# Optimization experiments

Measured on AMD Instinct MI355X. Metric: run time of the kernel, lower is better.

## Reference

```python
import jax, jax.numpy as jnp
import numpy as np

N_NODES = 50000
DEG = 16                      # uniform in-degree so every node receives messages (matches dgl mailbox semantics)
N_EDGES = N_NODES * DEG       # 800000
IND = 128
EDIM = 64
OUT = 128
AVG_D = float(np.log(DEG + 1.0))   # PNA avg_d['log']
EPS = 1e-5


def setup_inputs() -> dict:
    key = jax.random.key(0)
    k = jax.random.split(key, 6)
    h = jax.random.normal(k[0], (N_NODES, IND), dtype=jnp.float32)
    ef = jax.random.normal(k[1], (N_EDGES, EDIM), dtype=jnp.float32)
    src = jax.random.randint(k[2], (N_EDGES,), 0, N_NODES)
    dst = jnp.repeat(jnp.arange(N_NODES), DEG)  # every node has exactly DEG incoming edges
    pre_in = 2 * IND + EDIM            # 320
    post_in = IND * (1 + 4 * 3)        # 1664: h + 4 aggregators x 3 scalers
    W_pre = jax.random.normal(k[3], (pre_in, IND), dtype=jnp.float32) * (1.0 / np.sqrt(pre_in))
    b_pre = jnp.zeros((IND,), dtype=jnp.float32)
    W_post = jax.random.normal(k[4], (post_in, OUT), dtype=jnp.float32) * (1.0 / np.sqrt(post_in))
    b_post = jnp.zeros((OUT,), dtype=jnp.float32)
    return {"h": h, "ef": ef, "src": src, "dst": dst,
            "W_pre": W_pre, "b_pre": b_pre, "W_post": W_post, "b_post": b_post}


def reference(h, ef, src, dst, W_pre, b_pre, W_post, b_post):
    n = h.shape[0]
    # --- pretrans on edges: cat(src_h, dst_h, ef) -> Linear ---
    z2 = jnp.concatenate([h[src], h[dst], ef], axis=1)          # [E, 2*IND+EDIM]
    e = z2 @ W_pre + b_pre                                       # [E, IND]
    # --- multi-aggregator segment reduce over incoming edges (by dst) ---
    deg = jax.ops.segment_sum(jnp.ones((e.shape[0],), e.dtype), dst, num_segments=n)  # [N]
    safe_deg = jnp.maximum(deg, 1.0)[:, None]
    s1 = jax.ops.segment_sum(e, dst, num_segments=n)
    s2 = jax.ops.segment_sum(e * e, dst, num_segments=n)
    mean = s1 / safe_deg
    std = jnp.sqrt(jax.nn.relu(s2 / safe_deg - mean * mean) + EPS)
    mx = jax.ops.segment_max(e, dst, num_segments=n)
    mn = jax.ops.segment_min(e, dst, num_segments=n)
    has = (deg > 0)[:, None]
    mx = jnp.where(has, mx, 0.0)
    mn = jnp.where(has, mn, 0.0)
    agg = jnp.concatenate([mean, mx, mn, std], axis=1)           # [N, 4*IND]
    # --- scalers: identity, amplification log(D+1)/avg_d, attenuation avg_d/log(D+1) ---
    logd = jnp.log(deg + 1.0)
    amp = (logd / AVG_D)[:, None]
    att = (AVG_D / jnp.maximum(logd, 1e-6))[:, None]
    att = jnp.where(deg[:, None] > 0, att, 0.0)
    scaled = jnp.concatenate([agg, agg * amp, agg * att], axis=1)  # [N, 12*IND]
    # --- posttrans on nodes: cat(h, aggregated) -> Linear ---
    hcat = jnp.concatenate([h, scaled], axis=1)                  # [N, 13*IND]
    return hcat @ W_post + b_post                                # [N, OUT]
```

## Files before the change

kernel.cpp:

```cpp
#include <hip/hip_runtime.h>

#define N_NODES 50000
#define IND 128
#define EDIM 64

typedef __bf16 bf16x8 __attribute__((ext_vector_type(8)));
typedef float  f32x4  __attribute__((ext_vector_type(4)));
typedef unsigned short u16x8 __attribute__((ext_vector_type(8)));

__device__ __forceinline__ unsigned short f2bfu(float f) {
  __bf16 b = (__bf16)f;
  return __builtin_bit_cast(unsigned short, b);
}
__device__ __forceinline__ float bfu2f(unsigned short u) {
  __bf16 b = __builtin_bit_cast(__bf16, u);
  return (float)b;
}
__device__ __forceinline__ f32x4 mfma16(bf16x8 a, bf16x8 b, f32x4 c) {
  return __builtin_amdgcn_mfma_f32_16x16x32_bf16(a, b, c, 0, 0, 0);
}
__device__ __forceinline__ bf16x8 pack8(float4 a, float4 b) {
  bf16x8 r;
  r[0]=(__bf16)a.x; r[1]=(__bf16)a.y; r[2]=(__bf16)a.z; r[3]=(__bf16)a.w;
  r[4]=(__bf16)b.x; r[5]=(__bf16)b.y; r[6]=(__bf16)b.z; r[7]=(__bf16)b.w;
  return r;
}

__global__ __launch_bounds__(256) void pack_all(const float* W_pre, const float* W_post,
                                                const float* b_pre, const float* b_post,
                                                unsigned short* WpreF, unsigned short* WcF,
                                                unsigned short* WfoldF, float* bias2) {
  __shared__ float ldsW[16384];
  int b = blockIdx.x, t = threadIdx.x;
  if (b < 16) {
    for (int i = 0; i < 64; i++) {
      int idx = t + i * 256;
      int c = idx >> 7, col = idx & 127;
      float s = 0.f;
#pragma unroll
      for (int sc = 0; sc < 3; sc++)
#pragma unroll
      for (int st = 0; st < 3; st++)
          s += W_post[(size_t)(128 + sc * 512 + st * 128 + c) * 128 + col];
      ldsW[idx] = s;
    }
    __syncthreads();
    int col = t & 127, kh = t >> 7;
    for (int i = 0; i < 4; i++) {
      int k = b * 8 + i * 2 + kh;
      float a0 = W_post[(size_t)k * 128 + col], a1 = 0.f, a2 = 0.f, a3 = 0.f;
      const float* wb = W_pre + (size_t)(128 + k) * 128;
#pragma unroll 4
      for (int c = 0; c < 128; c += 4) {
        a0 = fmaf(wb[c],     ldsW[c * 128 + col], a0);
        a1 = fmaf(wb[c + 1], ldsW[(c + 1) * 128 + col], a1);
        a2 = fmaf(wb[c + 2], ldsW[(c + 2) * 128 + col], a2);
        a3 = fmaf(wb[c + 3], ldsW[(c + 3) * 128 + col], a3);
      }
      float acc = (a0 + a1) + (a2 + a3);
      int kb = k >> 5, j = k & 7, qq = (k >> 3) & 3;
      int lane = qq * 16 + (col & 15), ct = col >> 4;
      WfoldF[((size_t)(kb * 8 + ct) * 64 + lane) * 8 + j] = f2bfu(acc);
    }
    if (b == 0 && t < 128) {
      int col = t;
      float acc = b_post[col];
      for (int c = 0; c < 128; c++) acc = fmaf(b_pre[c], ldsW[c * 128 + col], acc);
      bias2[col] = acc;
    }
  } else {
    int idx = (b - 16) * 256 + t;
    if (idx < 16384) {
      int j = idx & 7, lane = (idx >> 3) & 63, ct = (idx >> 9) & 7, kb = idx >> 12;
      int k = kb * 32 + (lane >> 4) * 8 + j;
      int col = ct * 16 + (lane & 15);
      WpreF[idx] = f2bfu(W_pre[k * 128 + col]);
    } else if (idx < 24576) {
      int i = idx - 16384;
      int j = i & 7, lane = (i >> 3) & 63, ct = (i >> 9) & 7, kb = i >> 12;
      int k = kb * 32 + (lane >> 4) * 8 + j;
      int col = ct * 16 + (lane & 15);
      WcF[i] = f2bfu(W_pre[(256 + k) * 128 + col]);
    } else if (idx < 24576 + 65536) {
      int i = idx - 24576;
      int j = i & 7, lane = (i >> 3) & 63, ct = (i >> 9) & 7, kbr = i >> 12;
      int kb = kbr + 4;
      int p = kbr * 32 + ((lane >> 4) & 3) * 8 + j;
      int tt = p >> 7;
      int c = (p & 7) * 16 + ((p >> 3) & 15);
      int col = ct * 16 + (lane & 15);
      size_t r0 = 128 + (size_t)tt * 128 + c;
      float v = W_post[r0 * 128 + col] + W_post[(r0 + 512) * 128 + col] +
                W_post[(r0 + 1024) * 128 + col];
      WfoldF[((size_t)(kb * 8 + ct) * 64 + lane) * 8 + j] = f2bfu(v);
    }
  }
}

__global__ __launch_bounds__(256) void pre_gemm(const float* h, const unsigned short* WpreF,
                                                unsigned short* haB) {
  int lane = threadIdx.x & 63;
  int gw = blockIdx.x * 4 + (threadIdx.x >> 6);
  size_t base = (size_t)gw * 16;
  if (base >= N_NODES) return;
  int q = lane >> 4, c16 = lane & 15;
  f32x4 acc[8];
#pragma unroll
  for (int i = 0; i < 8; i++) acc[i] = (f32x4){0.f, 0.f, 0.f, 0.f};
#pragma unroll
  for (int kb = 0; kb < 4; kb++) {
    const float* hp = h + (base + c16) * 128 + kb * 32 + q * 8;
    float4 lo = *(const float4*)hp;
    float4 hi = *(const float4*)(hp + 4);
    bf16x8 a = pack8(lo, hi);
#pragma unroll
    for (int ct = 0; ct < 8; ct++) {
      bf16x8 b = *(const bf16x8*)(WpreF + ((size_t)(kb * 8 + ct) * 64 + lane) * 8);
      acc[ct] = mfma16(a, b, acc[ct]);
    }
  }
#pragma unroll
  for (int r = 0; r < 4; r++) {
    size_t row = base + q * 4 + r;
    u16x8 hv;
#pragma unroll
    for (int ct = 0; ct < 8; ct++) hv[ct] = f2bfu(acc[ct][r]);
    *(u16x8*)(haB + row * 128 + c16 * 8) = hv;
  }
}

__device__ __forceinline__ void node_stats(const f32x4* acc, const u16x8* G,
                                           int q, unsigned short* outp) {
  u16x8 ov;
#pragma unroll
  for (int ct = 0; ct < 8; ct++) {
    float sum = 0.f, s2 = 0.f, mx = -3.4e38f, mn = 3.4e38f;
#pragma unroll
    for (int r = 0; r < 4; r++) {
      float e = acc[ct][r] + bfu2f(G[r][ct]);
      sum += e; s2 = __builtin_fmaf(e, e, s2);
      mx = fmaxf(mx, e); mn = fminf(mn, e);
    }
    sum += __shfl_xor(sum, 16, 64); s2 += __shfl_xor(s2, 16, 64);
    mx = fmaxf(mx, __shfl_xor(mx, 16, 64)); mn = fminf(mn, __shfl_xor(mn, 16, 64));
    sum += __shfl_xor(sum, 32, 64); s2 += __shfl_xor(s2, 32, 64);
    mx = fmaxf(mx, __shfl_xor(mx, 32, 64)); mn = fminf(mn, __shfl_xor(mn, 32, 64));
    float mean = sum * 0.0625f;
    float var = fmaxf(s2 * 0.0625f - mean * mean, 0.f);
    float sd = sqrtf(var + 1e-5f);
    float v = (q == 0) ? mean : (q == 1) ? mx : (q == 2) ? mn : sd;
    ov[ct] = f2bfu(v);
  }
  *(u16x8*)outp = ov;
}

__global__ __launch_bounds__(512, 4) void edge_post(const float* ef, const int* src,
                                                    const unsigned short* haB,
                                                    const unsigned short* WcF,
                                                    const float* h,
                                                    const unsigned short* WfoldF,
                                                    const float* bias2, float* out) {
  __shared__ unsigned short ldsWc[8192];
  __shared__ unsigned short sAgg[16 * 512];
  {
    const int4* g = (const int4*)WcF;
    int4* l = (int4*)ldsWc;
#pragma unroll
    for (int i = 0; i < 2; i++) l[threadIdx.x + i * 512] = g[threadIdx.x + i * 512];
  }
  int lane = threadIdx.x & 63, wib = threadIdx.x >> 6;
  int q = lane >> 4, c16 = lane & 15;
  int pr = blockIdx.x * 8 + wib;
  int n0 = pr * 2;
  int srcv = src[pr * 32 + (lane & 31)];
  const float* ep0 = ef + ((size_t)n0 * 16 + c16) * 64 + q * 8;
  float4 E0a = *(const float4*)ep0;
  float4 E0b = *(const float4*)(ep0 + 4);
  float4 E0c = *(const float4*)(ep0 + 32);
  float4 E0d = *(const float4*)(ep0 + 36);
  const float* ep1 = ep0 + 1024;
  float4 E1a = *(const float4*)ep1;
  float4 E1b = *(const float4*)(ep1 + 4);
  float4 E1c = *(const float4*)(ep1 + 32);
  float4 E1d = *(const float4*)(ep1 + 36);
  u16x8 G0[4], G1[4];
#pragma unroll
  for (int r = 0; r < 4; r++) {
    int s = __shfl(srcv, q * 4 + r, 64);
    G0[r] = *(const u16x8*)(haB + (size_t)s * 128 + c16 * 8);
  }
#pragma unroll
  for (int r = 0; r < 4; r++) {
    int s = __shfl(srcv, 16 + q * 4 + r, 64);
    G1[r] = *(const u16x8*)(haB + (size_t)s * 128 + c16 * 8);
  }
  __syncthreads();
  {
    bf16x8 a0 = pack8(E0a, E0b), a1 = pack8(E0c, E0d);
    f32x4 acc[8];
#pragma unroll
    for (int ct = 0; ct < 8; ct++) {
      bf16x8 b = *(const bf16x8*)(ldsWc + ((size_t)ct * 64 + lane) * 8);
      acc[ct] = mfma16(a0, b, (f32x4){0.f, 0.f, 0.f, 0.f});
    }
#pragma unroll
    for (int ct = 0; ct < 8; ct++) {
      bf16x8 b = *(const bf16x8*)(ldsWc + ((size_t)(8 + ct) * 64 + lane) * 8);
      acc[ct] = mfma16(a1, b, acc[ct]);
    }
    node_stats(acc, G0, q, sAgg + (size_t)(wib * 2) * 512 + lane * 8);
  }
  {
    bf16x8 a0 = pack8(E1a, E1b), a1 = pack8(E1c, E1d);
    f32x4 acc[8];
#pragma unroll
    for (int ct = 0; ct < 8; ct++) {
      bf16x8 b = *(const bf16x8*)(ldsWc + ((size_t)ct * 64 + lane) * 8);
      acc[ct] = mfma16(a0, b, (f32x4){0.f, 0.f, 0.f, 0.f});
    }
#pragma unroll
    for (int ct = 0; ct < 8; ct++) {
      bf16x8 b = *(const bf16x8*)(ldsWc + ((size_t)(8 + ct) * 64 + lane) * 8);
      acc[ct] = mfma16(a1, b, acc[ct]);
    }
    node_stats(acc, G1, q, sAgg + (size_t)(wib * 2 + 1) * 512 + lane * 8);
  }
  __syncthreads();
  size_t base = (size_t)blockIdx.x * 16;
  size_t r0 = base + c16;
  f32x4 acc = (f32x4){0.f, 0.f, 0.f, 0.f};
  float4 fa, fb;
  {
    const float* p = h + r0 * 128 + q * 8;
    fa = *(const float4*)p; fb = *(const float4*)(p + 4);
  }
  bf16x8 Bc = *(const bf16x8*)(WfoldF + ((size_t)wib * 64 + lane) * 8);
#pragma unroll
  for (int kb = 0; kb < 20; kb++) {
    bf16x8 a;
    if (kb < 4) {
      a = pack8(fa, fb);
      if (kb < 3) {
        const float* p = h + r0 * 128 + (kb + 1) * 32 + q * 8;
        fa = *(const float4*)p; fb = *(const float4*)(p + 4);
      }
    } else {
      a = *(const bf16x8*)(sAgg + (size_t)c16 * 512 + (kb - 4) * 32 + q * 8);
    }
    bf16x8 Bn = Bc;
    if (kb < 19)
      Bn = *(const bf16x8*)(WfoldF + ((size_t)((kb + 1) * 8 + wib) * 64 + lane) * 8);
    acc = mfma16(a, Bc, acc);
    Bc = Bn;
  }
  int col = wib * 16 + c16;
  float bp = bias2[col];
#pragma unroll
  for (int r = 0; r < 4; r++) {
    size_t row = base + q * 4 + r;
    out[row * 128 + col] = acc[r] + bp;
  }
}

extern "C" void kernel_launch(void* const* d_in, const int* in_sizes, int n_in,
                              void* d_out, int out_size, void* d_ws, size_t ws_size,
                              hipStream_t stream) {
  const float* h      = (const float*)d_in[0];
  const float* ef     = (const float*)d_in[1];
  const int*   src    = (const int*)d_in[2];
  const float* W_pre  = (const float*)d_in[4];
  const float* b_pre  = (const float*)d_in[5];
  const float* W_post = (const float*)d_in[6];
  const float* b_post = (const float*)d_in[7];
  float* out = (float*)d_out;

  char* ws = (char*)d_ws;
  unsigned short* haB    = (unsigned short*)ws;
  unsigned short* WpreF  = haB + (size_t)N_NODES * 128;
  unsigned short* WcF    = WpreF + 16384;
  unsigned short* WfoldF = WcF + 8192;
  float*          bias2  = (float*)(WfoldF + 81920);
  (void)in_sizes; (void)n_in; (void)out_size; (void)ws_size;

  pack_all<<<368, 256, 0, stream>>>(W_pre, W_post, b_pre, b_post, WpreF, WcF, WfoldF, bias2);
  pre_gemm<<<782, 256, 0, stream>>>(h, WpreF, haB);
  edge_post<<<3125, 512, 0, stream>>>(ef, src, haB, WcF, h, WfoldF, bias2, out);
}
```

Measured before the change: 397.5 us.

## Use permlane swaps for node stats, swizzle aggregate LDS, vectorize src loads

Replaces the shuffle-based cross-lane reductions in node_stats with permlane32/permlane16 swap builtins. It packs sum/sumsq and max/negated-min into shared exchanges so fewer cross-lane operations are issued. The aggregate buffer in LDS is re-laid out with an XOR swizzle so the posttrans reads avoid bank conflicts. Source indices now come from vectorized int4 loads instead of per-lane shuffles, and the W_fold prefetch is deepened to two stages. The swap-based reduction is intricate and depends on the builtins being available, otherwise the old path is compiled.

Result: faster. 389.4 us (-2.0%).

```diff
diff --git a/kernel.cpp b/kernel.cpp
--- a/kernel.cpp
+++ b/kernel.cpp
@@ -15,6 +15,12 @@
 __device__ __forceinline__ float bfu2f(unsigned short u) {
   __bf16 b = __builtin_bit_cast(__bf16, u);
   return (float)b;
+}
+__device__ __forceinline__ unsigned int f2i(float f) {
+  return __builtin_bit_cast(unsigned int, f);
+}
+__device__ __forceinline__ float i2f(unsigned int u) {
+  return __builtin_bit_cast(float, u);
 }
 __device__ __forceinline__ f32x4 mfma16(bf16x8 a, bf16x8 b, f32x4 c) {
   return __builtin_amdgcn_mfma_f32_16x16x32_bf16(a, b, c, 0, 0, 0);
@@ -129,6 +135,47 @@
   }
 }
 
+#if __has_builtin(__builtin_amdgcn_permlane32_swap) && __has_builtin(__builtin_amdgcn_permlane16_swap)
+typedef unsigned int u32x2 __attribute__((ext_vector_type(2)));
+__device__ __forceinline__ void node_stats(const f32x4* acc, const u16x8* G,
+                                           int q, unsigned short* outp) {
+  int oddq = q & 1;
+  u16x8 ov;
+#pragma unroll
+  for (int ct = 0; ct < 8; ct++) {
+    float sum = 0.f, s2 = 0.f, mx = -3.4e38f, nmn = -3.4e38f;
+#pragma unroll
+    for (int r = 0; r < 4; r++) {
+      float e = acc[ct][r] + bfu2f(G[r][ct]);
+      sum += e; s2 = __builtin_fmaf(e, e, s2);
+      mx = fmaxf(mx, e); nmn = fmaxf(nmn, -e);
+    }
+    u32x2 pA = __builtin_amdgcn_permlane32_swap(f2i(sum), f2i(s2), false, false);
+    float t1 = i2f(pA[0]) + i2f(pA[1]);
+    u32x2 pB = __builtin_amdgcn_permlane32_swap(f2i(mx), f2i(nmn), false, false);
+    float t2 = fmaxf(i2f(pB[0]), i2f(pB[1]));
+    u32x2 pC = __builtin_amdgcn_permlane16_swap(f2i(t1), f2i(t2), false, false);
+    float d = i2f(pC[0]), s = i2f(pC[1]);
+    float u = oddq ? fmaxf(d, s) : (d + s);
+    u32x2 pD = __builtin_amdgcn_permlane16_swap(f2i(u), f2i(u), false, false);
+    u32x2 pE = __builtin_amdgcn_permlane32_swap(pD[0], pD[0], false, false);
+    float d2 = i2f(pD[0]);
+    float sv = i2f(pD[1]);
+    float d3 = i2f(pE[0]);
+    float v;
+    if (q == 0)      v = u * 0.0625f;
+    else if (q == 1) v = u;
+    else if (q == 2) v = -sv;
+    else {
+      float m = d3 * 0.0625f;
+      float var = fmaxf(d2 * 0.0625f - m * m, 0.f);
+      v = sqrtf(var + 1e-5f);
+    }
+    ov[ct] = f2bfu(v);
+  }
+  *(u16x8*)outp = ov;
+}
+#else
 __device__ __forceinline__ void node_stats(const f32x4* acc, const u16x8* G,
                                            int q, unsigned short* outp) {
   u16x8 ov;
@@ -153,6 +200,7 @@
   }
   *(u16x8*)outp = ov;
 }
+#endif
 
 __global__ __launch_bounds__(512, 4) void edge_post(const float* ef, const int* src,
                                                     const unsigned short* haB,
@@ -172,7 +220,9 @@
   int q = lane >> 4, c16 = lane & 15;
   int pr = blockIdx.x * 8 + wib;
   int n0 = pr * 2;
-  int srcv = src[pr * 32 + (lane & 31)];
+  const int4* s4p = (const int4*)src + (size_t)pr * 8;
+  int4 sv0 = s4p[q];
+  int4 sv1 = s4p[4 + q];
   const float* ep0 = ef + ((size_t)n0 * 16 + c16) * 64 + q * 8;
   float4 E0a = *(const float4*)ep0;
   float4 E0b = *(const float4*)(ep0 + 4);
@@ -184,16 +234,14 @@
   float4 E1c = *(const float4*)(ep1 + 32);
   float4 E1d = *(const float4*)(ep1 + 36);
   u16x8 G0[4], G1[4];
-#pragma unroll
-  for (int r = 0; r < 4; r++) {
-    int s = __shfl(srcv, q * 4 + r, 64);
-    G0[r] = *(const u16x8*)(haB + (size_t)s * 128 + c16 * 8);
-  }
-#pragma unroll
-  for (int r = 0; r < 4; r++) {
-    int s = __shfl(srcv, 16 + q * 4 + r, 64);
-    G1[r] = *(const u16x8*)(haB + (size_t)s * 128 + c16 * 8);
-  }
+  G0[0] = *(const u16x8*)(haB + (size_t)sv0.x * 128 + c16 * 8);
+  G0[1] = *(const u16x8*)(haB + (size_t)sv0.y * 128 + c16 * 8);
+  G0[2] = *(const u16x8*)(haB + (size_t)sv0.z * 128 + c16 * 8);
+  G0[3] = *(const u16x8*)(haB + (size_t)sv0.w * 128 + c16 * 8);
+  G1[0] = *(const u16x8*)(haB + (size_t)sv1.x * 128 + c16 * 8);
+  G1[1] = *(const u16x8*)(haB + (size_t)sv1.y * 128 + c16 * 8);
+  G1[2] = *(const u16x8*)(haB + (size_t)sv1.z * 128 + c16 * 8);
+  G1[3] = *(const u16x8*)(haB + (size_t)sv1.w * 128 + c16 * 8);
   __syncthreads();
   {
     bf16x8 a0 = pack8(E0a, E0b), a1 = pack8(E0c, E0d);
@@ -208,7 +256,8 @@
       bf16x8 b = *(const bf16x8*)(ldsWc + ((size_t)(8 + ct) * 64 + lane) * 8);
       acc[ct] = mfma16(a1, b, acc[ct]);
     }
-    node_stats(acc, G0, q, sAgg + (size_t)(wib * 2) * 512 + lane * 8);
+    node_stats(acc, G0, q,
+               sAgg + ((size_t)lane * 16 + ((wib * 2) ^ (lane & 15))) * 8);
   }
   {
     bf16x8 a0 = pack8(E1a, E1b), a1 = pack8(E1c, E1d);
@@ -223,7 +272,8 @@
       bf16x8 b = *(const bf16x8*)(ldsWc + ((size_t)(8 + ct) * 64 + lane) * 8);
       acc[ct] = mfma16(a1, b, acc[ct]);
     }
-    node_stats(acc, G1, q, sAgg + (size_t)(wib * 2 + 1) * 512 + lane * 8);
+    node_stats(acc, G1, q,
+               sAgg + ((size_t)lane * 16 + ((wib * 2 + 1) ^ (lane & 15))) * 8);
   }
   __syncthreads();
   size_t base = (size_t)blockIdx.x * 16;
@@ -234,7 +284,8 @@
     const float* p = h + r0 * 128 + q * 8;
     fa = *(const float4*)p; fb = *(const float4*)(p + 4);
   }
-  bf16x8 Bc = *(const bf16x8*)(WfoldF + ((size_t)wib * 64 + lane) * 8);
+  bf16x8 B0 = *(const bf16x8*)(WfoldF + ((size_t)(0 * 8 + wib) * 64 + lane) * 8);
+  bf16x8 B1 = *(const bf16x8*)(WfoldF + ((size_t)(1 * 8 + wib) * 64 + lane) * 8);
 #pragma unroll
   for (int kb = 0; kb < 20; kb++) {
     bf16x8 a;
@@ -245,13 +296,14 @@
         fa = *(const float4*)p; fb = *(const float4*)(p + 4);
       }
     } else {
-      a = *(const bf16x8*)(sAgg + (size_t)c16 * 512 + (kb - 4) * 32 + q * 8);
-    }
-    bf16x8 Bn = Bc;
-    if (kb < 19)
-      Bn = *(const bf16x8*)(WfoldF + ((size_t)((kb + 1) * 8 + wib) * 64 + lane) * 8);
-    acc = mfma16(a, Bc, acc);
-    Bc = Bn;
+      int chunk = (kb - 4) * 4 + q;
+      a = *(const bf16x8*)(sAgg + ((size_t)chunk * 16 + (c16 ^ (chunk & 15))) * 8);
+    }
+    bf16x8 Bn = B0;
+    if (kb + 2 < 20)
+      Bn = *(const bf16x8*)(WfoldF + ((size_t)((kb + 2) * 8 + wib) * 64 + lane) * 8);
+    acc = mfma16(a, B0, acc);
+    B0 = B1; B1 = Bn;
   }
   int col = wib * 16 + c16;
   float bp = bias2[col];
```
